# Optimization experiments

Measured on AMD Instinct MI355X. Metric: run time of the kernel, lower is better.

The kernel has to match this reference:

```python
import jax, jax.numpy as jnp
import numpy as np

N = 10000      # nodes
E = 320000     # edges (before self-loops)
D_IN = 256
HID = 128
HEADS = 4
D_OUT = 256
SLOPE = 0.2    # PyG GATConv default negative_slope


def setup_inputs() -> dict:
    key = jax.random.key(0)
    ks = jax.random.split(key, 10)
    s = 0.05
    return {
        "x": jax.random.normal(ks[0], (N, D_IN), dtype=jnp.float32),
        "edge_index": jax.random.randint(ks[1], (2, E), 0, N),
        # layer 1: in=256 -> heads=4, out=128, concat
        "W1": jax.random.normal(ks[2], (D_IN, HEADS * HID), dtype=jnp.float32) * s,
        "a1_src": jax.random.normal(ks[3], (HEADS, HID), dtype=jnp.float32) * s,
        "a1_dst": jax.random.normal(ks[4], (HEADS, HID), dtype=jnp.float32) * s,
        "b1": jax.random.normal(ks[5], (HEADS * HID,), dtype=jnp.float32) * s,
        # layer 2: in=512 -> heads=1, out=256, no concat
        "W2": jax.random.normal(ks[6], (HEADS * HID, D_OUT), dtype=jnp.float32) * s,
        "a2_src": jax.random.normal(ks[7], (1, D_OUT), dtype=jnp.float32) * s,
        "a2_dst": jax.random.normal(ks[8], (1, D_OUT), dtype=jnp.float32) * s,
        "b2": jax.random.normal(ks[9], (D_OUT,), dtype=jnp.float32) * s,
    }


def gat_conv(x, src, dst, W, a_src, a_dst, bias, heads, out_dim, concat):
    """PyG-style GATConv (eval mode, self-loops pre-added to src/dst)."""
    n = x.shape[0]
    h = (x @ W).reshape(n, heads, out_dim)            # [N, H, F]
    # per-edge attention logits: LeakyReLU(a_src.h_src + a_dst.h_dst)
    as_n = (h * a_src).sum(-1)                         # [N, H]
    ad_n = (h * a_dst).sum(-1)                         # [N, H]
    logit = jax.nn.leaky_relu(as_n[src] + ad_n[dst], negative_slope=SLOPE)  # [E, H]
    # segment softmax over edges grouped by destination node
    logit = logit - jax.ops.segment_max(logit, dst, num_segments=n)[dst]
    ex = jnp.exp(logit)
    alpha = ex / jax.ops.segment_sum(ex, dst, num_segments=n)[dst]          # [E, H]
    # weighted scatter-aggregation of source messages
    out = jax.ops.segment_sum(h[src] * alpha[:, :, None], dst, num_segments=n)  # [N, H, F]
    out = out.reshape(n, heads * out_dim) if concat else out.mean(axis=1)
    return out + bias


def reference(x, edge_index, W1, a1_src, a1_dst, b1, W2, a2_src, a2_dst, b2):
    # add self-loops once (PyG GATConv default add_self_loops=True)
    loops = jnp.arange(N, dtype=edge_index.dtype)
    src = jnp.concatenate([edge_index[0], loops])
    dst = jnp.concatenate([edge_index[1], loops])
    h = gat_conv(x, src, dst, W1, a1_src, a1_dst, b1, HEADS, HID, True)
    h = jax.nn.elu(h)  # dropout is identity at eval
    return gat_conv(h, src, dst, W2, a2_src, a2_dst, b2, 1, D_OUT, False)
```

## Files before the change

kernel.cpp:

```cpp
#include <hip/hip_runtime.h>

#define N_NODES 10000
#define E_RAW   320000
#define E_TOT   330000
#define D_IN    256
#define HID     128
#define HEADS   4
#define F1      512
#define D_OUT   256
#define SLOPE   0.2f
#define EBLOCKS 1290

typedef __attribute__((ext_vector_type(8))) short bf16x8;
typedef __attribute__((ext_vector_type(4))) float f32x4;

__device__ __forceinline__ float bf2f(ushort u) {
    return __uint_as_float(((uint)u) << 16);
}
__device__ __forceinline__ ushort f2bf(float x) {
    uint u = __float_as_uint(x);
    uint r = (u + 0x7FFFu + ((u >> 16) & 1u)) >> 16;
    return (ushort)r;
}
__device__ __forceinline__ float bfu_lo(uint u) { return __uint_as_float(u << 16); }
__device__ __forceinline__ float bfu_hi(uint u) { return __uint_as_float(u & 0xFFFF0000u); }

__device__ __forceinline__ void gload_lds16(const void* g, void* l) {
    __builtin_amdgcn_global_load_lds(
        (const __attribute__((address_space(1))) void*)g,
        (__attribute__((address_space(3))) void*)l, 16, 0, 0);
}


__global__ __launch_bounds__(256) void k_zero_all(int* __restrict__ deg,
                                                  float* __restrict__ as1,
                                                  float* __restrict__ ad1,
                                                  float* __restrict__ as2,
                                                  float* __restrict__ ad2) {
    int i = blockIdx.x * 256 + threadIdx.x;
    if (i < 4 * N_NODES) { as1[i] = 0.f; ad1[i] = 0.f; }
    if (i < N_NODES) { deg[i] = 0; as2[i] = 0.f; ad2[i] = 0.f; }
}


__global__ __launch_bounds__(256) void k_hist(const int* __restrict__ ei, int* __restrict__ deg) {
    int e = blockIdx.x * 256 + threadIdx.x;
    if (e < E_TOT) {
        int dst = (e < E_RAW) ? ei[E_RAW + e] : (e - E_RAW);
        atomicAdd(&deg[dst], 1);
    }
}


#define SCAN_CHUNK 40

__global__ __launch_bounds__(256) void k_prep(const int* __restrict__ deg,
                                              int* __restrict__ row_start,
                                              int* __restrict__ cursor,
                                              const float* __restrict__ W1,
                                              ushort* __restrict__ w1h,
                                              const float* __restrict__ W2,
                                              ushort* __restrict__ w2h,
                                              const float* __restrict__ x,
                                              ushort* __restrict__ xb) {
    int b = blockIdx.x;
    int tid = threadIdx.x;
    if (b == 0) {
        __shared__ int tots[256];
        int base = tid * SCAN_CHUNK;
        int loc[SCAN_CHUNK];
        int s = 0;
        #pragma unroll
        for (int k = 0; k < SCAN_CHUNK; k++) {
            int idx = base + k;
            int v = (idx < N_NODES) ? deg[idx] : 0;
            loc[k] = s;
            s += v;
        }
        tots[tid] = s;
        __syncthreads();
        for (int off = 1; off < 256; off <<= 1) {
            int t = (tid >= off) ? tots[tid - off] : 0;
            __syncthreads();
            tots[tid] += t;
            __syncthreads();
        }
        int excl = tots[tid] - s;
        #pragma unroll
        for (int k = 0; k < SCAN_CHUNK; k++) {
            int idx = base + k;
            if (idx < N_NODES) {
                int r = excl + loc[k];
                row_start[idx] = r;
                cursor[idx]    = r;
            }
        }
        if (tid == 255) row_start[N_NODES] = E_TOT;
    } else if (b <= 64) {
        int task = (b - 1) * 4 + (tid >> 6);
        int lane = tid & 63;
        int n = (task >> 5) * 64 + lane;
        int k0 = (task & 31) * 8;
        float v[8];
        #pragma unroll
        for (int j = 0; j < 8; j++) v[j] = W1[(size_t)(k0 + j) * F1 + n];
        uint4 u;
        u.x = (uint)f2bf(v[0]) | ((uint)f2bf(v[1]) << 16);
        u.y = (uint)f2bf(v[2]) | ((uint)f2bf(v[3]) << 16);
        u.z = (uint)f2bf(v[4]) | ((uint)f2bf(v[5]) << 16);
        u.w = (uint)f2bf(v[6]) | ((uint)f2bf(v[7]) << 16);
        *(uint4*)&w1h[(size_t)n * D_IN + k0] = u;
    } else if (b <= 128) {
        int task = (b - 65) * 4 + (tid >> 6);
        int lane = tid & 63;
        int n = (task >> 6) * 64 + lane;
        int k0 = (task & 63) * 8;
        float v[8];
        #pragma unroll
        for (int j = 0; j < 8; j++) v[j] = W2[(size_t)(k0 + j) * D_OUT + n];
        uint4 u;
        u.x = (uint)f2bf(v[0]) | ((uint)f2bf(v[1]) << 16);
        u.y = (uint)f2bf(v[2]) | ((uint)f2bf(v[3]) << 16);
        u.z = (uint)f2bf(v[4]) | ((uint)f2bf(v[5]) << 16);
        u.w = (uint)f2bf(v[6]) | ((uint)f2bf(v[7]) << 16);
        *(uint4*)&w2h[(size_t)n * F1 + k0] = u;
    } else {
        int i8 = (b - 129) * 256 + tid;
        float4 a = *(const float4*)&x[(size_t)i8 * 8];
        float4 c = *(const float4*)&x[(size_t)i8 * 8 + 4];
        uint4 u;
        u.x = (uint)f2bf(a.x) | ((uint)f2bf(a.y) << 16);
        u.y = (uint)f2bf(a.z) | ((uint)f2bf(a.w) << 16);
        u.z = (uint)f2bf(c.x) | ((uint)f2bf(c.y) << 16);
        u.w = (uint)f2bf(c.z) | ((uint)f2bf(c.w) << 16);
        *(uint4*)&xb[(size_t)i8 * 8] = u;
    }
}


__global__ __launch_bounds__(256) void k_scatter(const int* __restrict__ ei,
                                                 int* __restrict__ cursor,
                                                 int* __restrict__ csr_src) {
    int e = blockIdx.x * 256 + threadIdx.x;
    if (e < E_TOT) {
        int src = (e < E_RAW) ? ei[e] : (e - E_RAW);
        int dst = (e < E_RAW) ? ei[E_RAW + e] : (e - E_RAW);
        int pos = atomicAdd(&cursor[dst], 1);
        csr_src[pos] = src;
    }
}


template<int BM, int KD, int ND, int WC, int HMUL>
__device__ __forceinline__ void gemm_attn(int bx, int by, int tid,
                                          const ushort* __restrict__ A,
                                          const ushort* __restrict__ B,
                                          ushort* __restrict__ C,
                                          const float* __restrict__ avs,
                                          const float* __restrict__ avd,
                                          float* __restrict__ os,
                                          float* __restrict__ od) {
    constexpr int WR = 4 / WC;
    constexpr int MI = (BM / WR) / 16;
    constexpr int NJ = (64 / WC) / 16;
    constexpr int NT = KD / 64;
    __shared__ ushort sA[2][BM * 64];
    __shared__ ushort sB[2][64 * 64];

    const int lane = tid & 63;
    const int wid = tid >> 6;
    const int wr = wid / WC;
    const int wc = wid % WC;
    const int m0 = by * BM;
    const int n0 = bx * 64;
    const int fr = lane & 15;
    const int fs = lane >> 4;
    const int rowc = lane >> 3;
    const int slot = (lane & 7) ^ rowc;

    f32x4 acc[MI][NJ];
    #pragma unroll
    for (int i = 0; i < MI; i++)
        #pragma unroll
        for (int j = 0; j < NJ; j++) acc[i][j] = (f32x4){0.f, 0.f, 0.f, 0.f};

    auto STAGE = [&](int buf, int k0) {
        #pragma unroll
        for (int t = 0; t < BM / 32; t++) {
            int c = wid + 4 * t;
            int gr = m0 + c * 8 + rowc;
            gr = gr < N_NODES ? gr : N_NODES - 1;
            gload_lds16(A + (size_t)gr * KD + k0 + slot * 8, &sA[buf][c * 512]);
        }
        #pragma unroll
        for (int t = 0; t < 2; t++) {
            int c = wid + 4 * t;
            gload_lds16(B + (size_t)(n0 + c * 8 + rowc) * KD + k0 + slot * 8, &sB[buf][c * 512]);
        }
    };
    auto COMPUTE = [&](int buf) {
        #pragma unroll
        for (int kk = 0; kk < 2; kk++) {
            int sbase = kk * 4 + fs;
            bf16x8 a_f[MI], b_f[NJ];
            #pragma unroll
            for (int i = 0; i < MI; i++) {
                int r = wr * 64 + i * 16 + fr;
                a_f[i] = *(const bf16x8*)&sA[buf][r * 64 + ((sbase ^ (r & 7)) << 3)];
            }
            #pragma unroll
            for (int j = 0; j < NJ; j++) {
                int cc = wc * (64 / WC) + j * 16 + fr;
                b_f[j] = *(const bf16x8*)&sB[buf][cc * 64 + ((sbase ^ (cc & 7)) << 3)];
            }
            #pragma unroll
            for (int i = 0; i < MI; i++)
                #pragma unroll
                for (int j = 0; j < NJ; j++)
                    acc[i][j] = __builtin_amdgcn_mfma_f32_16x16x32_bf16(a_f[i], b_f[j], acc[i][j], 0, 0, 0);
        }
    };

    STAGE(0, 0);
    __syncthreads();
    int cur = 0;
    #pragma unroll
    for (int t = 0; t < NT - 1; t++) {
        STAGE(cur ^ 1, (t + 1) * 64);
        COMPUTE(cur);
        __syncthreads();
        cur ^= 1;
    }
    COMPUTE(cur);

    const int hoff = (HMUL == 4) ? (n0 >> 7) : 0;
    float sv[NJ], dv[NJ];
    int cols[NJ];
    #pragma unroll
    for (int j = 0; j < NJ; j++) {
        cols[j] = n0 + wc * (64 / WC) + j * 16 + fr;
        sv[j] = avs[cols[j]];
        dv[j] = avd[cols[j]];
    }
    #pragma unroll
    for (int i = 0; i < MI; i++) {
        int row_base = m0 + wr * 64 + i * 16 + (fs << 2);
        float ps[4], pd[4];
        #pragma unroll
        for (int q = 0; q < 4; q++) {
            int r = row_base + q;
            float p_s = 0.f, p_d = 0.f;
            #pragma unroll
            for (int j = 0; j < NJ; j++) {
                float v = acc[i][j][q];
                if (r < N_NODES) C[(size_t)r * ND + cols[j]] = f2bf(v);
                p_s += v * sv[j];
                p_d += v * dv[j];
            }
            ps[q] = p_s; pd[q] = p_d;
        }
        #pragma unroll
        for (int q = 0; q < 4; q++) {
            #pragma unroll
            for (int m = 8; m >= 1; m >>= 1) {
                ps[q] += __shfl_xor(ps[q], m, 16);
                pd[q] += __shfl_xor(pd[q], m, 16);
            }
        }
        if (fr == 0) {
            #pragma unroll
            for (int q = 0; q < 4; q++) {
                int r = row_base + q;
                if (r < N_NODES) {
                    atomicAdd(&os[r * HMUL + hoff], ps[q]);
                    atomicAdd(&od[r * HMUL + hoff], pd[q]);
                }
            }
        }
    }
}


__global__ __launch_bounds__(256) void k_gemm1(const ushort* __restrict__ xb,
                                               const ushort* __restrict__ w1h,
                                               ushort* __restrict__ h1,
                                               const float* __restrict__ a1s,
                                               const float* __restrict__ a1d,
                                               float* __restrict__ as1,
                                               float* __restrict__ ad1) {
    int g = blockIdx.x;
    gemm_attn<128, D_IN, F1, 2, 4>(g % 8, g / 8, threadIdx.x,
                                   xb, w1h, h1, a1s, a1d, as1, ad1);
}


__global__ __launch_bounds__(256) void k_gemm2(const ushort* __restrict__ heluh,
                                               const ushort* __restrict__ w2h,
                                               ushort* __restrict__ h2,
                                               const float* __restrict__ a2s,
                                               const float* __restrict__ a2d,
                                               float* __restrict__ as2,
                                               float* __restrict__ ad2) {
    int b = blockIdx.x;
    gemm_attn<64, F1, D_OUT, 4, 1>(b % 4, b / 4, threadIdx.x,
                                   heluh, w2h, h2, a2s, a2d, as2, ad2);
}


__device__ __forceinline__ void fma8(uint4 v, float e, float* acc) {
    acc[0] += bfu_lo(v.x) * e; acc[1] += bfu_hi(v.x) * e;
    acc[2] += bfu_lo(v.y) * e; acc[3] += bfu_hi(v.y) * e;
    acc[4] += bfu_lo(v.z) * e; acc[5] += bfu_hi(v.z) * e;
    acc[6] += bfu_lo(v.w) * e; acc[7] += bfu_hi(v.w) * e;
}

__global__ __launch_bounds__(256) void k_edge1(const int* __restrict__ row_start,
                                               const int* __restrict__ csr_src,
                                               const ushort* __restrict__ h1,
                                               const float* __restrict__ as1,
                                               const float* __restrict__ ad1,
                                               const float* __restrict__ b1,
                                               ushort* __restrict__ heluh) {
    int node = blockIdx.x * 4 + (threadIdx.x >> 6);
    int lane = threadIdx.x & 63;
    int start = row_start[node];
    int end   = row_start[node + 1];
    int h_lane = lane >> 4;

    float adl = ad1[node * 4 + h_lane];

    float acc[8] = {0,0,0,0,0,0,0,0};
    float sum = 0.f;
    const size_t lo8 = (size_t)lane * 8;

    int i = start;
    for (; i + 8 <= end; i += 8) {
        int s[8];
        #pragma unroll
        for (int k = 0; k < 8; k++) s[k] = csr_src[i + k];
        float l[8];
        #pragma unroll
        for (int k = 0; k < 8; k++) l[k] = as1[s[k] * 4 + h_lane];
        uint4 v[8];
        #pragma unroll
        for (int k = 0; k < 8; k++) v[k] = *(const uint4*)(h1 + (size_t)s[k] * F1 + lo8);
        #pragma unroll
        for (int k = 0; k < 8; k++) {
            float t = l[k] + adl;
            t = t > 0.f ? t : SLOPE * t;
            float e = __expf(t);
            sum += e;
            fma8(v[k], e, acc);
        }
    }
    for (; i < end; i++) {
        int s0 = csr_src[i];
        float t = as1[s0 * 4 + h_lane] + adl;
        uint4 v0 = *(const uint4*)(h1 + (size_t)s0 * F1 + lo8);
        t = t > 0.f ? t : SLOPE * t;
        float e = __expf(t);
        sum += e;
        fma8(v0, e, acc);
    }
    float inv = 1.f / sum;

    size_t o = (size_t)node * F1 + lo8;
    const float* bp = b1 + lo8;
    uint pk[4];
    #pragma unroll
    for (int j = 0; j < 4; j++) {
        float v0 = acc[2*j]   * inv + bp[2*j];
        float v1 = acc[2*j+1] * inv + bp[2*j+1];
        v0 = v0 > 0.f ? v0 : (__expf(v0) - 1.f);
        v1 = v1 > 0.f ? v1 : (__expf(v1) - 1.f);
        pk[j] = (uint)f2bf(v0) | ((uint)f2bf(v1) << 16);
    }
    *(uint4*)&heluh[o] = make_uint4(pk[0], pk[1], pk[2], pk[3]);
}

__global__ __launch_bounds__(256) void k_edge2(const int* __restrict__ row_start,
                                               const int* __restrict__ csr_src,
                                               const ushort* __restrict__ h2,
                                               const float* __restrict__ as2,
                                               const float* __restrict__ ad2,
                                               const float* __restrict__ b2,
                                               float* __restrict__ out) {
    int node = blockIdx.x * 4 + (threadIdx.x >> 6);
    int lane = threadIdx.x & 63;
    int sub = lane >> 5;
    int fl  = lane & 31;
    int start = row_start[node];
    int end   = row_start[node + 1];

    float ad = ad2[node];

    float acc[8] = {0,0,0,0,0,0,0,0};
    float sum = 0.f;
    const size_t fo = (size_t)fl * 8;

    int i = start;
    for (; i + 8 <= end; i += 8) {
        int s[4];
        #pragma unroll
        for (int k = 0; k < 4; k++) s[k] = csr_src[i + 2 * k + sub];
        float l[4];
        #pragma unroll
        for (int k = 0; k < 4; k++) l[k] = as2[s[k]];
        uint4 v[4];
        #pragma unroll
        for (int k = 0; k < 4; k++) v[k] = *(const uint4*)(h2 + (size_t)s[k] * D_OUT + fo);
        #pragma unroll
        for (int k = 0; k < 4; k++) {
            float t = l[k] + ad;
            t = t > 0.f ? t : SLOPE * t;
            float e = __expf(t);
            sum += e;
            fma8(v[k], e, acc);
        }
    }
    for (; i < end; i += 2) {
        if (i + sub < end) {
            int s0 = csr_src[i + sub];
            float t = as2[s0] + ad;
            uint4 v0 = *(const uint4*)(h2 + (size_t)s0 * D_OUT + fo);
            t = t > 0.f ? t : SLOPE * t;
            float e = __expf(t);
            sum += e;
            fma8(v0, e, acc);
        }
    }
    #pragma unroll
    for (int j = 0; j < 8; j++) acc[j] += __shfl_xor(acc[j], 32, 64);
    sum += __shfl_xor(sum, 32, 64);
    float inv = 1.f / sum;

    if (lane < 32) {
        size_t o = (size_t)node * D_OUT + fo;
        const float* bp = b2 + fo;
        float4 r0, r1;
        r0.x = acc[0] * inv + bp[0]; r0.y = acc[1] * inv + bp[1];
        r0.z = acc[2] * inv + bp[2]; r0.w = acc[3] * inv + bp[3];
        r1.x = acc[4] * inv + bp[4]; r1.y = acc[5] * inv + bp[5];
        r1.z = acc[6] * inv + bp[6]; r1.w = acc[7] * inv + bp[7];
        *(float4*)&out[o] = r0;
        *(float4*)&out[o + 4] = r1;
    }
}


extern "C" void kernel_launch(void* const* d_in, const int* in_sizes, int n_in,
                              void* d_out, int out_size, void* d_ws, size_t ws_size,
                              hipStream_t stream) {
    const float* x   = (const float*)d_in[0];
    const int*   ei  = (const int*)d_in[1];
    const float* W1  = (const float*)d_in[2];
    const float* a1s = (const float*)d_in[3];
    const float* a1d = (const float*)d_in[4];
    const float* b1  = (const float*)d_in[5];
    const float* W2  = (const float*)d_in[6];
    const float* a2s = (const float*)d_in[7];
    const float* a2d = (const float*)d_in[8];
    const float* b2  = (const float*)d_in[9];
    float* out = (float*)d_out;

    char* ws = (char*)d_ws;
    size_t off = 0;
    auto take = [&](size_t bytes) {
        char* p = ws + off;
        off += (bytes + 255) & ~(size_t)255;
        return p;
    };
    int*    deg       = (int*)take(sizeof(int) * N_NODES);
    int*    row_start = (int*)take(sizeof(int) * (N_NODES + 1));
    int*    cursor    = (int*)take(sizeof(int) * N_NODES);
    int*    csr_src   = (int*)take(sizeof(int) * E_TOT);
    ushort* xb        = (ushort*)take(sizeof(ushort) * (size_t)N_NODES * D_IN);
    ushort* w1h       = (ushort*)take(sizeof(ushort) * D_IN * F1);
    ushort* w2h       = (ushort*)take(sizeof(ushort) * F1 * D_OUT);
    ushort* h1        = (ushort*)take(sizeof(ushort) * (size_t)N_NODES * F1);
    float*  as1       = (float*)take(sizeof(float) * N_NODES * 4);
    float*  ad1       = (float*)take(sizeof(float) * N_NODES * 4);
    ushort* heluh     = (ushort*)take(sizeof(ushort) * (size_t)N_NODES * F1);
    ushort* h2        = (ushort*)take(sizeof(ushort) * (size_t)N_NODES * D_OUT);
    float*  as2       = (float*)take(sizeof(float) * N_NODES);
    float*  ad2       = (float*)take(sizeof(float) * N_NODES);

    k_zero_all<<<(4 * N_NODES + 255) / 256, 256, 0, stream>>>(deg, as1, ad1, as2, ad2);
    k_hist<<<EBLOCKS, 256, 0, stream>>>(ei, deg);
    k_prep<<<1379, 256, 0, stream>>>(deg, row_start, cursor, W1, w1h, W2, w2h, x, xb);
    k_scatter<<<EBLOCKS, 256, 0, stream>>>(ei, cursor, csr_src);
    k_gemm1<<<8 * 79, 256, 0, stream>>>(xb, w1h, h1, a1s, a1d, as1, ad1);
    k_edge1<<<N_NODES / 4, 256, 0, stream>>>(row_start, csr_src, h1, as1, ad1, b1, heluh);
    k_gemm2<<<4 * 157, 256, 0, stream>>>(heluh, w2h, h2, a2s, a2d, as2, ad2);
    k_edge2<<<N_NODES / 4, 256, 0, stream>>>(row_start, csr_src, h2, as2, ad2, b2, out);
}
```

Before: 175.7 us.

## Record atomic ranks in histogram, single-buffer GEMM, split edge1 nodes across two waves

The histogram kernel now stores each edge's atomic rank, so the scatter kernel writes to row_start[dst]+rank without a second atomic pass and the cursor array goes away. The GEMM drops its LDS double buffer for a simple load-sync-compute loop, which halves LDS use but gives up overlap of loads with MFMA. The layer-1 edge kernel now uses two waves per node, with half-waves taking alternating edges, and combines their results with a cross-lane shuffle. This doubles the parallelism of the gather but adds a reduction step and leaves half the lanes idle during output.

```diff
diff --git a/kernel.cpp b/kernel.cpp
--- a/kernel.cpp
+++ b/kernel.cpp
@@ -5,11 +5,11 @@
 #define E_TOT   330000
 #define D_IN    256
 #define HID     128
-#define HEADS   4
 #define F1      512
 #define D_OUT   256
 #define SLOPE   0.2f
 #define EBLOCKS 1290
+#define SCAN_CHUNK 40
 
 typedef __attribute__((ext_vector_type(8))) short bf16x8;
 typedef __attribute__((ext_vector_type(4))) float f32x4;
@@ -43,20 +43,19 @@
 }
 
 
-__global__ __launch_bounds__(256) void k_hist(const int* __restrict__ ei, int* __restrict__ deg) {
+__global__ __launch_bounds__(256) void k_hist(const int* __restrict__ ei,
+                                              int* __restrict__ deg,
+                                              int* __restrict__ rank) {
     int e = blockIdx.x * 256 + threadIdx.x;
     if (e < E_TOT) {
         int dst = (e < E_RAW) ? ei[E_RAW + e] : (e - E_RAW);
-        atomicAdd(&deg[dst], 1);
-    }
-}
-
-
-#define SCAN_CHUNK 40
+        rank[e] = atomicAdd(&deg[dst], 1);
+    }
+}
+
 
 __global__ __launch_bounds__(256) void k_prep(const int* __restrict__ deg,
                                               int* __restrict__ row_start,
-                                              int* __restrict__ cursor,
                                               const float* __restrict__ W1,
                                               ushort* __restrict__ w1h,
                                               const float* __restrict__ W2,
@@ -89,11 +88,7 @@
         #pragma unroll
         for (int k = 0; k < SCAN_CHUNK; k++) {
             int idx = base + k;
-            if (idx < N_NODES) {
-                int r = excl + loc[k];
-                row_start[idx] = r;
-                cursor[idx]    = r;
-            }
+            if (idx < N_NODES) row_start[idx] = excl + loc[k];
         }
         if (tid == 255) row_start[N_NODES] = E_TOT;
     } else if (b <= 64) {
@@ -139,14 +134,14 @@
 
 
 __global__ __launch_bounds__(256) void k_scatter(const int* __restrict__ ei,
-                                                 int* __restrict__ cursor,
+                                                 const int* __restrict__ row_start,
+                                                 const int* __restrict__ rank,
                                                  int* __restrict__ csr_src) {
     int e = blockIdx.x * 256 + threadIdx.x;
     if (e < E_TOT) {
         int src = (e < E_RAW) ? ei[e] : (e - E_RAW);
         int dst = (e < E_RAW) ? ei[E_RAW + e] : (e - E_RAW);
-        int pos = atomicAdd(&cursor[dst], 1);
-        csr_src[pos] = src;
+        csr_src[row_start[dst] + rank[e]] = src;
     }
 }
 
@@ -163,9 +158,8 @@
     constexpr int WR = 4 / WC;
     constexpr int MI = (BM / WR) / 16;
     constexpr int NJ = (64 / WC) / 16;
-    constexpr int NT = KD / 64;
-    __shared__ ushort sA[2][BM * 64];
-    __shared__ ushort sB[2][64 * 64];
+    __shared__ ushort sA[BM * 64];
+    __shared__ ushort sB[64 * 64];
 
     const int lane = tid & 63;
     const int wid = tid >> 6;
@@ -184,21 +178,20 @@
         #pragma unroll
         for (int j = 0; j < NJ; j++) acc[i][j] = (f32x4){0.f, 0.f, 0.f, 0.f};
 
-    auto STAGE = [&](int buf, int k0) {
+    for (int k0 = 0; k0 < KD; k0 += 64) {
         #pragma unroll
         for (int t = 0; t < BM / 32; t++) {
             int c = wid + 4 * t;
             int gr = m0 + c * 8 + rowc;
             gr = gr < N_NODES ? gr : N_NODES - 1;
-            gload_lds16(A + (size_t)gr * KD + k0 + slot * 8, &sA[buf][c * 512]);
+            gload_lds16(A + (size_t)gr * KD + k0 + slot * 8, &sA[c * 512]);
         }
         #pragma unroll
         for (int t = 0; t < 2; t++) {
             int c = wid + 4 * t;
-            gload_lds16(B + (size_t)(n0 + c * 8 + rowc) * KD + k0 + slot * 8, &sB[buf][c * 512]);
-        }
-    };
-    auto COMPUTE = [&](int buf) {
+            gload_lds16(B + (size_t)(n0 + c * 8 + rowc) * KD + k0 + slot * 8, &sB[c * 512]);
+        }
+        __syncthreads();
         #pragma unroll
         for (int kk = 0; kk < 2; kk++) {
             int sbase = kk * 4 + fs;
@@ -206,12 +199,12 @@
             #pragma unroll
             for (int i = 0; i < MI; i++) {
                 int r = wr * 64 + i * 16 + fr;
-                a_f[i] = *(const bf16x8*)&sA[buf][r * 64 + ((sbase ^ (r & 7)) << 3)];
+                a_f[i] = *(const bf16x8*)&sA[r * 64 + ((sbase ^ (r & 7)) << 3)];
             }
             #pragma unroll
             for (int j = 0; j < NJ; j++) {
                 int cc = wc * (64 / WC) + j * 16 + fr;
-                b_f[j] = *(const bf16x8*)&sB[buf][cc * 64 + ((sbase ^ (cc & 7)) << 3)];
+                b_f[j] = *(const bf16x8*)&sB[cc * 64 + ((sbase ^ (cc & 7)) << 3)];
             }
             #pragma unroll
             for (int i = 0; i < MI; i++)
@@ -219,19 +212,8 @@
                 for (int j = 0; j < NJ; j++)
                     acc[i][j] = __builtin_amdgcn_mfma_f32_16x16x32_bf16(a_f[i], b_f[j], acc[i][j], 0, 0, 0);
         }
-    };
-
-    STAGE(0, 0);
-    __syncthreads();
-    int cur = 0;
-    #pragma unroll
-    for (int t = 0; t < NT - 1; t++) {
-        STAGE(cur ^ 1, (t + 1) * 64);
-        COMPUTE(cur);
         __syncthreads();
-        cur ^= 1;
-    }
-    COMPUTE(cur);
+    }
 
     const int hoff = (HMUL == 4) ? (n0 >> 7) : 0;
     float sv[NJ], dv[NJ];
@@ -279,7 +261,6 @@
         }
     }
 }
-
 
 __global__ __launch_bounds__(256) void k_gemm1(const ushort* __restrict__ xb,
                                                const ushort* __restrict__ w1h,
@@ -293,7 +274,6 @@
                                    xb, w1h, h1, a1s, a1d, as1, ad1);
 }
 
-
 __global__ __launch_bounds__(256) void k_gemm2(const ushort* __restrict__ heluh,
                                                const ushort* __restrict__ w2h,
                                                ushort* __restrict__ h2,
@@ -321,31 +301,34 @@
                                                const float* __restrict__ ad1,
                                                const float* __restrict__ b1,
                                                ushort* __restrict__ heluh) {
-    int node = blockIdx.x * 4 + (threadIdx.x >> 6);
+    int node = blockIdx.x * 2 + (threadIdx.x >> 7);
+    int wid2 = (threadIdx.x >> 6) & 1;
     int lane = threadIdx.x & 63;
+    int sub  = lane >> 5;
+    int fl   = lane & 31;
     int start = row_start[node];
     int end   = row_start[node + 1];
-    int h_lane = lane >> 4;
-
-    float adl = ad1[node * 4 + h_lane];
+
+    const int fb   = wid2 * 256 + fl * 8;
+    const int head = fb >> 7;
+    float adl = ad1[node * 4 + head];
 
     float acc[8] = {0,0,0,0,0,0,0,0};
     float sum = 0.f;
-    const size_t lo8 = (size_t)lane * 8;
 
     int i = start;
     for (; i + 8 <= end; i += 8) {
-        int s[8];
-        #pragma unroll
-        for (int k = 0; k < 8; k++) s[k] = csr_src[i + k];
-        float l[8];
-        #pragma unroll
-        for (int k = 0; k < 8; k++) l[k] = as1[s[k] * 4 + h_lane];
-        uint4 v[8];
-        #pragma unroll
-        for (int k = 0; k < 8; k++) v[k] = *(const uint4*)(h1 + (size_t)s[k] * F1 + lo8);
-        #pragma unroll
-        for (int k = 0; k < 8; k++) {
+        int s[4];
+        #pragma unroll
+        for (int k = 0; k < 4; k++) s[k] = csr_src[i + 2 * k + sub];
+        float l[4];
+        #pragma unroll
+        for (int k = 0; k < 4; k++) l[k] = as1[s[k] * 4 + head];
+        uint4 v[4];
+        #pragma unroll
+        for (int k = 0; k < 4; k++) v[k] = *(const uint4*)(h1 + (size_t)s[k] * F1 + fb);
+        #pragma unroll
+        for (int k = 0; k < 4; k++) {
             float t = l[k] + adl;
             t = t > 0.f ? t : SLOPE * t;
             float e = __expf(t);
@@ -353,29 +336,36 @@
             fma8(v[k], e, acc);
         }
     }
-    for (; i < end; i++) {
-        int s0 = csr_src[i];
-        float t = as1[s0 * 4 + h_lane] + adl;
-        uint4 v0 = *(const uint4*)(h1 + (size_t)s0 * F1 + lo8);
-        t = t > 0.f ? t : SLOPE * t;
-        float e = __expf(t);
-        sum += e;
-        fma8(v0, e, acc);
-    }
+    for (; i < end; i += 2) {
+        if (i + sub < end) {
+            int s0 = csr_src[i + sub];
+            float t = as1[s0 * 4 + head] + adl;
+            uint4 v0 = *(const uint4*)(h1 + (size_t)s0 * F1 + fb);
+            t = t > 0.f ? t : SLOPE * t;
+            float e = __expf(t);
+            sum += e;
+            fma8(v0, e, acc);
+        }
+    }
+    #pragma unroll
+    for (int j = 0; j < 8; j++) acc[j] += __shfl_xor(acc[j], 32, 64);
+    sum += __shfl_xor(sum, 32, 64);
     float inv = 1.f / sum;
 
-    size_t o = (size_t)node * F1 + lo8;
-    const float* bp = b1 + lo8;
-    uint pk[4];
-    #pragma unroll
-    for (int j = 0; j < 4; j++) {
-        float v0 = acc[2*j]   * inv + bp[2*j];
-        float v1 = acc[2*j+1] * inv + bp[2*j+1];
-        v0 = v0 > 0.f ? v0 : (__expf(v0) - 1.f);
-        v1 = v1 > 0.f ? v1 : (__expf(v1) - 1.f);
-        pk[j] = (uint)f2bf(v0) | ((uint)f2bf(v1) << 16);
-    }
-    *(uint4*)&heluh[o] = make_uint4(pk[0], pk[1], pk[2], pk[3]);
+    if (lane < 32) {
+        size_t o = (size_t)node * F1 + fb;
+        const float* bp = b1 + fb;
+        uint pk[4];
+        #pragma unroll
+        for (int j = 0; j < 4; j++) {
+            float v0 = acc[2*j]   * inv + bp[2*j];
+            float v1 = acc[2*j+1] * inv + bp[2*j+1];
+            v0 = v0 > 0.f ? v0 : (__expf(v0) - 1.f);
+            v1 = v1 > 0.f ? v1 : (__expf(v1) - 1.f);
+            pk[j] = (uint)f2bf(v0) | ((uint)f2bf(v1) << 16);
+        }
+        *(uint4*)&heluh[o] = make_uint4(pk[0], pk[1], pk[2], pk[3]);
+    }
 }
 
 __global__ __launch_bounds__(256) void k_edge2(const int* __restrict__ row_start,
@@ -393,7 +383,6 @@
     int end   = row_start[node + 1];
 
     float ad = ad2[node];
-
     float acc[8] = {0,0,0,0,0,0,0,0};
     float sum = 0.f;
     const size_t fo = (size_t)fl * 8;
@@ -471,8 +460,8 @@
         return p;
     };
     int*    deg       = (int*)take(sizeof(int) * N_NODES);
+    int*    rank      = (int*)take(sizeof(int) * E_TOT);
     int*    row_start = (int*)take(sizeof(int) * (N_NODES + 1));
-    int*    cursor    = (int*)take(sizeof(int) * N_NODES);
     int*    csr_src   = (int*)take(sizeof(int) * E_TOT);
     ushort* xb        = (ushort*)take(sizeof(ushort) * (size_t)N_NODES * D_IN);
     ushort* w1h       = (ushort*)take(sizeof(ushort) * D_IN * F1);
@@ -486,11 +475,11 @@
     float*  ad2       = (float*)take(sizeof(float) * N_NODES);
 
     k_zero_all<<<(4 * N_NODES + 255) / 256, 256, 0, stream>>>(deg, as1, ad1, as2, ad2);
-    k_hist<<<EBLOCKS, 256, 0, stream>>>(ei, deg);
-    k_prep<<<1379, 256, 0, stream>>>(deg, row_start, cursor, W1, w1h, W2, w2h, x, xb);
-    k_scatter<<<EBLOCKS, 256, 0, stream>>>(ei, cursor, csr_src);
+    k_hist<<<EBLOCKS, 256, 0, stream>>>(ei, deg, rank);
+    k_prep<<<1379, 256, 0, stream>>>(deg, row_start, W1, w1h, W2, w2h, x, xb);
+    k_scatter<<<EBLOCKS, 256, 0, stream>>>(ei, row_start, rank, csr_src);
     k_gemm1<<<8 * 79, 256, 0, stream>>>(xb, w1h, h1, a1s, a1d, as1, ad1);
-    k_edge1<<<N_NODES / 4, 256, 0, stream>>>(row_start, csr_src, h1, as1, ad1, b1, heluh);
+    k_edge1<<<N_NODES / 2, 256, 0, stream>>>(row_start, csr_src, h1, as1, ad1, b1, heluh);
     k_gemm2<<<4 * 157, 256, 0, stream>>>(heluh, w2h, h2, a2s, a2d, as2, ad2);
     k_edge2<<<N_NODES / 4, 256, 0, stream>>>(row_start, csr_src, h2, as2, ad2, b2, out);
 }
```

Measured after the change: 153.7 us. 1.14x faster.
